# Kernel tuning notes

Measured on AMD Instinct MI355X. Metric: run time of the kernel, lower is better.

## Reference

```python
import jax, jax.numpy as jnp
import numpy as np

B, N, K, DIM = 1, 50000, 16, 64


def setup_inputs() -> dict:
    key = jax.random.key(0)
    ks = jax.random.split(key, 16)
    s = 0.05  # weight init scale
    return {
        "points_xyz": jax.random.normal(ks[0], (B, N, 3), jnp.float32),
        "points_features": jax.random.normal(ks[1], (B, N, DIM), jnp.float32),
        "neighbours_xyz": jax.random.normal(ks[2], (B, N, K, 3), jnp.float32),
        "neighbours_features": jax.random.normal(ks[3], (B, N, K, DIM), jnp.float32),
        "W_phi": jax.random.normal(ks[4], (DIM, DIM), jnp.float32) * s,
        "b_phi": jnp.zeros((DIM,), jnp.float32),
        "W_psi": jax.random.normal(ks[5], (DIM, DIM), jnp.float32) * s,
        "b_psi": jnp.zeros((DIM,), jnp.float32),
        "W_alpha": jax.random.normal(ks[6], (DIM, DIM), jnp.float32) * s,
        "b_alpha": jnp.zeros((DIM,), jnp.float32),
        "W_gamma": jax.random.normal(ks[7], (DIM, DIM), jnp.float32) * s,
        "b_gamma": jnp.zeros((DIM,), jnp.float32),
        "W_d1": jax.random.normal(ks[8], (3, DIM), jnp.float32) * s,
        "b_d1": jnp.zeros((DIM,), jnp.float32),
        "W_d2": jax.random.normal(ks[9], (DIM, DIM), jnp.float32) * s,
        "b_d2": jnp.zeros((DIM,), jnp.float32),
    }


def reference(points_xyz, points_features, neighbours_xyz, neighbours_features,
              W_phi, b_phi, W_psi, b_psi, W_alpha, b_alpha, W_gamma, b_gamma,
              W_d1, b_d1, W_d2, b_d2):
    # Positional encoding: delta(p_i - p_j) -> (B, N, K, DIM)
    diff = points_xyz[:, :, None, :] - neighbours_xyz          # (B,N,K,3)
    delta = jax.nn.relu((diff @ W_d1 + b_d1) @ W_d2 + b_d2)    # (B,N,K,DIM)

    phi = (points_features @ W_phi + b_phi)[:, :, None, :]     # (B,N,1,DIM)
    psi = neighbours_features @ W_psi + b_psi                  # (B,N,K,DIM)
    beta = phi - psi + delta                                   # (B,N,K,DIM)

    gamma_out = beta @ W_gamma + b_gamma                       # (B,N,K,DIM)
    # NOTE: faithful to source: softmax over the FEATURE axis (dim=-1)
    rho = jax.nn.softmax(gamma_out, axis=-1)                   # (B,N,K,DIM)

    alpha_out = neighbours_features @ W_alpha + b_alpha + delta  # (B,N,K,DIM)
    out = jnp.sum(rho * alpha_out, axis=2)                     # (B,N,DIM)
    return out
```

## Files before the change

### kernel.cpp

```cpp
#include <hip/hip_runtime.h>
#include <hip/hip_bf16.h>

typedef unsigned int uint_t;
typedef __attribute__((ext_vector_type(8))) short bf16x8;
typedef __attribute__((ext_vector_type(4))) float f32x4;

#define NPTS 50000
#define DIM  64
#define KNB  16
#define GPW  8
#define NGROUPS (NPTS / GPW)
#define WPB  4
#define NBLOCKS ((NGROUPS + WPB - 1) / WPB)

#define FR_WA    0
#define FR_PSIG  2048
#define FR_WG    4096
#define FR_PHIG  6144
#define WC4      8192
#define GB       8448
#define BA       8512

__device__ __forceinline__ uint_t pk(float a, float b) {
    union { __hip_bfloat162 h; uint_t u; } cv;
    cv.h = __float22bfloat162_rn(float2{a, b});
    return cv.u;
}

union Frag { uint_t u[4]; bf16x8 s; uint4 v; };

__device__ __forceinline__ int sigma(int k) {
    int t = k >> 1;
    return (t & 15) + 32 * (t >> 4) + 16 * (k & 1);
}

__global__ void pt_prep(const float* __restrict__ Wphi, const float* __restrict__ bphi,
                        const float* __restrict__ Wpsi, const float* __restrict__ bpsi,
                        const float* __restrict__ Wa,   const float* __restrict__ ba,
                        const float* __restrict__ Wg,   const float* __restrict__ bg,
                        const float* __restrict__ Wd1,  const float* __restrict__ bd1,
                        const float* __restrict__ Wd2,  const float* __restrict__ bd2,
                        float* __restrict__ ws) {
    int b = blockIdx.x, t = threadIdx.x;
    uint_t* wsu = (uint_t*)ws;
    if (b < 32) {
        int gid  = b * 256 + t;
        int img  = gid >> 11;
        int rem  = gid & 2047;
        int f    = rem >> 8;
        int lane = (rem >> 2) & 63;
        int w    = rem & 3;
        int k0   = (f & 1) * 32 + (lane >> 4) * 8 + 2 * w;
        int k1   = k0 + 1;
        int n    = (f >> 1) * 16 + (lane & 15);
        float v0, v1;
        if (img == 0) {
            v0 = Wa[k0 * 64 + n]; v1 = Wa[k1 * 64 + n];
            wsu[FR_WA + rem] = pk(v0, v1);
        } else if (img == 1) {
            float a0 = 0.f, a1 = 0.f;
            for (int c = 0; c < 64; ++c) {
                float wgc = Wg[c * 64 + n];
                a0 += Wpsi[k0 * 64 + c] * wgc;
                a1 += Wpsi[k1 * 64 + c] * wgc;
            }
            wsu[FR_PSIG + rem] = pk(-a0, -a1);
        } else if (img == 2) {
            v0 = Wg[sigma(k0) * 64 + n]; v1 = Wg[sigma(k1) * 64 + n];
            wsu[FR_WG + rem] = pk(v0, v1);
        } else {
            float a0 = 0.f, a1 = 0.f;
            for (int c = 0; c < 64; ++c) {
                float wgc = Wg[c * 64 + n];
                a0 += Wphi[k0 * 64 + c] * wgc;
                a1 += Wphi[k1 * 64 + c] * wgc;
            }
            wsu[FR_PHIG + rem] = pk(a0, a1);
        }
    } else if (t < 64) {
        float wx = 0.f, wy = 0.f, wz = 0.f;
        for (int m = 0; m < 64; ++m) {
            float w2 = Wd2[m * 64 + t];
            wx += Wd1[m] * w2;
            wy += Wd1[64 + m] * w2;
            wz += Wd1[128 + m] * w2;
        }
        float wb = bd2[t];
        for (int m = 0; m < 64; ++m) wb += bd1[m] * Wd2[m * 64 + t];
        ws[WC4 + t * 4 + 0] = wx;
        ws[WC4 + t * 4 + 1] = wy;
        ws[WC4 + t * 4 + 2] = wz;
        ws[WC4 + t * 4 + 3] = wb;
        float g = bg[t];
        for (int c = 0; c < 64; ++c) g += (bphi[c] - bpsi[c]) * Wg[c * 64 + t];
        ws[GB + t] = g;
        ws[BA + t] = ba[t];
    }
}

#define MFMA(A, B, C) __builtin_amdgcn_mfma_f32_16x16x32_bf16((A), (B), (C), 0, 0, 0)

#define O_PHIG 0
#define O_UTR  520
#define O_DXY  1064
#define O_PXY  1128
#define O_OBUF 1160
#define O_NF   1672
#define NFSLOT 1088
#define WAREA  (O_NF + 3 * NFSLOT)

__device__ __forceinline__ void gl_lds16(const void* g, void* l) {
    __builtin_amdgcn_global_load_lds(
        (const __attribute__((address_space(1))) unsigned int*)g,
        (__attribute__((address_space(3))) unsigned int*)l, 16, 0, 0);
}
__device__ __forceinline__ void gl_lds4(const void* g, void* l) {
    __builtin_amdgcn_global_load_lds(
        (const __attribute__((address_space(1))) unsigned int*)g,
        (__attribute__((address_space(3))) unsigned int*)l, 4, 0, 0);
}

__device__ __forceinline__ void stage_pt(const float* __restrict__ nfeat,
                                         const float* __restrict__ nxyz,
                                         int p, float* ldsbase,
                                         const int* soff, int lane) {
    const char* sp = (const char*)nfeat + (size_t)p * 4096;
    gl_lds16(sp + soff[0], ldsbase);
    gl_lds16(sp + soff[1], ldsbase + 256);
    gl_lds16(sp + soff[2], ldsbase + 512);
    gl_lds16(sp + soff[3], ldsbase + 768);
    int xi = p * 48 + lane;
    if (xi > NPTS * KNB * 3 - 1) xi = NPTS * KNB * 3 - 1;
    gl_lds4(nxyz + xi, ldsbase + 1024);
}

__global__ __launch_bounds__(256, 2)
void pt_main(const float* __restrict__ pxyz, const float* __restrict__ pfeat,
             const float* __restrict__ nxyz, const float* __restrict__ nfeat,
             const float* __restrict__ ws,   float* __restrict__ out) {
    __shared__ float lds[WPB][WAREA];

    const int t    = threadIdx.x;
    const int wv   = t >> 6;
    const int lane = t & 63;
    const int c16  = lane & 15;
    const int quad = lane >> 4;

    const int g = blockIdx.x * WPB + wv;
    if (g >= NGROUPS) return;

    float*  W      = lds[wv];
    float*  phig_s = W + O_PHIG;
    uint_t* utr    = (uint_t*)(W + O_UTR);
    float*  dxyz   = W + O_DXY;
    float*  pxyz_s = W + O_PXY;
    float*  obuf   = W + O_OBUF;
    float*  nfl    = W + O_NF;

    const int g0 = g * GPW;
    const int k3 = lane / 3, c3 = lane - k3 * 3;

    int soff[4];
    #pragma unroll
    for (int j = 0; j < 4; ++j) {
        int row = j * 4 + quad;
        soff[j] = row * 256 + (((c16 - row) & 15) << 4);
    }

    stage_pt(nfeat, nxyz, g0,     nfl + 0 * NFSLOT, soff, lane);
    stage_pt(nfeat, nxyz, g0 + 1, nfl + 1 * NFSLOT, soff, lane);

    const uint4* fr = (const uint4*)ws;
    Frag wa[8], wpsig[8], wg[8];
    #pragma unroll
    for (int f = 0; f < 8; ++f) {
        wa[f].v    = fr[        f * 64 + lane];
        wpsig[f].v = fr[ 512 +  f * 64 + lane];
        wg[f].v    = fr[1024 +  f * 64 + lane];
    }
    float4 wc[4];
    float ba_r[4], gbr[4];
    #pragma unroll
    for (int nt = 0; nt < 4; ++nt) {
        int d = nt * 16 + c16;
        wc[nt]   = ((const float4*)(ws + WC4))[d];
        ba_r[nt] = ws[BA + d];
        gbr[nt]  = ws[GB + d];
    }

    if (lane < 24) pxyz_s[lane] = pxyz[g0 * 3 + lane];

    {
        float4 x0{}, x1{}, x2{}, x3{};
        if (c16 < 8) {
            const float* base = pfeat + (size_t)(g0 + c16) * 64 + quad * 8;
            x0 = *(const float4*)(base);
            x1 = *(const float4*)(base + 4);
            x2 = *(const float4*)(base + 32);
            x3 = *(const float4*)(base + 36);
        }
        Frag pa0, pa1;
        pa0.u[0] = pk(x0.x, x0.y); pa0.u[1] = pk(x0.z, x0.w);
        pa0.u[2] = pk(x1.x, x1.y); pa0.u[3] = pk(x1.z, x1.w);
        pa1.u[0] = pk(x2.x, x2.y); pa1.u[1] = pk(x2.z, x2.w);
        pa1.u[2] = pk(x3.x, x3.y); pa1.u[3] = pk(x3.z, x3.w);
        #pragma unroll
        for (int nt = 0; nt < 4; ++nt) {
            Frag b0, b1;
            b0.v = fr[1536 + (nt * 2 + 0) * 64 + lane];
            b1.v = fr[1536 + (nt * 2 + 1) * 64 + lane];
            f32x4 acc = {gbr[nt], gbr[nt], gbr[nt], gbr[nt]};
            acc = MFMA(pa0.s, b0.s, acc);
            acc = MFMA(pa1.s, b1.s, acc);
            if (quad < 2) {
                #pragma unroll
                for (int r = 0; r < 4; ++r)
                    phig_s[(quad * 4 + r) * 65 + nt * 16 + c16] = acc[r];
            }
        }
    }

    int slot = 0;
    #pragma unroll 1
    for (int i = 0; i < GPW; ++i) {
        const int n = g0 + i;

        if (i + 2 < GPW) {
            int s2 = slot + 2; if (s2 >= 3) s2 -= 3;
            stage_pt(nfeat, nxyz, n + 2, nfl + s2 * NFSLOT, soff, lane);
        }
        __builtin_amdgcn_sched_barrier(0);
        if (i < GPW - 2)       { asm volatile("s_waitcnt vmcnt(10)" ::: "memory"); }
        else if (i == GPW - 2) { asm volatile("s_waitcnt vmcnt(5)"  ::: "memory"); }
        else                   { asm volatile("s_waitcnt vmcnt(0)"  ::: "memory"); }
        __builtin_amdgcn_sched_barrier(0);

        const float* nfp = nfl + slot * NFSLOT;

        if (lane < 48) {
            float v = nfp[1024 + lane];
            dxyz[k3 * 4 + c3] = pxyz_s[i * 3 + c3] - v;
        }

        int b0 = c16 * 64 + (((quad * 2     + c16) & 15) << 2);
        int b1 = c16 * 64 + (((quad * 2 + 1 + c16) & 15) << 2);
        int b2 = c16 * 64 + (((quad * 2 + 8 + c16) & 15) << 2);
        int b3 = c16 * 64 + (((quad * 2 + 9 + c16) & 15) << 2);
        float4 x0 = *(const float4*)(nfp + b0);
        float4 x1 = *(const float4*)(nfp + b1);
        float4 x2 = *(const float4*)(nfp + b2);
        float4 x3 = *(const float4*)(nfp + b3);
        Frag na0, na1;
        na0.u[0] = pk(x0.x, x0.y); na0.u[1] = pk(x0.z, x0.w);
        na0.u[2] = pk(x1.x, x1.y); na0.u[3] = pk(x1.z, x1.w);
        na1.u[0] = pk(x2.x, x2.y); na1.u[1] = pk(x2.z, x2.w);
        na1.u[2] = pk(x3.x, x3.y); na1.u[3] = pk(x3.z, x3.w);

        float ph[4];
        #pragma unroll
        for (int nt = 0; nt < 4; ++nt) ph[nt] = phig_s[i * 65 + nt * 16 + c16];
        float4 dd[4];
        #pragma unroll
        for (int r = 0; r < 4; ++r)
            dd[r] = ((const float4*)dxyz)[quad * 4 + r];

        float d_c[4][4];
        #pragma unroll
        for (int nt = 0; nt < 4; ++nt) {
            #pragma unroll
            for (int r = 0; r < 4; ++r) {
                float u = fmaf(dd[r].x, wc[nt].x,
                          fmaf(dd[r].y, wc[nt].y,
                          fmaf(dd[r].z, wc[nt].z, wc[nt].w)));
                d_c[nt][r] = fmaxf(u, 0.f);
            }
        }
        #pragma unroll
        for (int r = 0; r < 4; ++r) {
            int row = (quad * 4 + r) * 34;
            utr[row + c16]      = pk(d_c[0][r], d_c[1][r]);
            utr[row + 16 + c16] = pk(d_c[2][r], d_c[3][r]);
        }

        f32x4 aacc[4];
        #pragma unroll
        for (int nt = 0; nt < 4; ++nt) {
            aacc[nt] = f32x4{ba_r[nt], ba_r[nt], ba_r[nt], ba_r[nt]};
            aacc[nt] = MFMA(na0.s, wa[nt * 2 + 0].s, aacc[nt]);
            aacc[nt] = MFMA(na1.s, wa[nt * 2 + 1].s, aacc[nt]);
        }
        f32x4 gacc[4];
        #pragma unroll
        for (int nt = 0; nt < 4; ++nt) {
            gacc[nt] = f32x4{ph[nt], ph[nt], ph[nt], ph[nt]};
            gacc[nt] = MFMA(na0.s, wpsig[nt * 2 + 0].s, gacc[nt]);
            gacc[nt] = MFMA(na1.s, wpsig[nt * 2 + 1].s, gacc[nt]);
        }
        Frag da0, da1;
        {
            const uint_t* rowp = utr + c16 * 34 + quad * 4;
            uint2 a = *(const uint2*)(rowp);
            uint2 b = *(const uint2*)(rowp + 2);
            uint2 c = *(const uint2*)(rowp + 16);
            uint2 d = *(const uint2*)(rowp + 18);
            da0.u[0] = a.x; da0.u[1] = a.y; da0.u[2] = b.x; da0.u[3] = b.y;
            da1.u[0] = c.x; da1.u[1] = c.y; da1.u[2] = d.x; da1.u[3] = d.y;
        }
        #pragma unroll
        for (int nt = 0; nt < 4; ++nt) {
            gacc[nt] = MFMA(da0.s, wg[nt * 2 + 0].s, gacc[nt]);
            gacc[nt] = MFMA(da1.s, wg[nt * 2 + 1].s, gacc[nt]);
        }
        #pragma unroll
        for (int nt = 0; nt < 4; ++nt)
            #pragma unroll
            for (int r = 0; r < 4; ++r) aacc[nt][r] += d_c[nt][r];

        float e[4][4], smi[4];
        #pragma unroll
        for (int r = 0; r < 4; ++r) {
            float s = 0.f;
            #pragma unroll
            for (int nt = 0; nt < 4; ++nt) { e[nt][r] = __expf(gacc[nt][r]); s += e[nt][r]; }
            #pragma unroll
            for (int d2 = 1; d2 < 16; d2 <<= 1) s += __shfl_xor(s, d2);
            smi[r] = __builtin_amdgcn_rcpf(s);
        }
        float p0 = 0.f, p1 = 0.f, p2 = 0.f, p3 = 0.f;
        #pragma unroll
        for (int r = 0; r < 4; ++r) {
            p0 = fmaf(e[0][r] * smi[r], aacc[0][r], p0);
            p1 = fmaf(e[1][r] * smi[r], aacc[1][r], p1);
            p2 = fmaf(e[2][r] * smi[r], aacc[2][r], p2);
            p3 = fmaf(e[3][r] * smi[r], aacc[3][r], p3);
        }
        p0 += __shfl_xor(p0, 16); p0 += __shfl_xor(p0, 32);
        p1 += __shfl_xor(p1, 16); p1 += __shfl_xor(p1, 32);
        p2 += __shfl_xor(p2, 16); p2 += __shfl_xor(p2, 32);
        p3 += __shfl_xor(p3, 16); p3 += __shfl_xor(p3, 32);
        float sel = (quad == 0) ? p0 : (quad == 1) ? p1 : (quad == 2) ? p2 : p3;
        obuf[i * 64 + lane] = sel;

        slot = (slot == 2) ? 0 : slot + 1;
    }

    float4 o0 = ((const float4*)obuf)[lane * 2];
    float4 o1 = ((const float4*)obuf)[lane * 2 + 1];
    float4* og = (float4*)(out + (size_t)g0 * 64);
    og[lane * 2]     = o0;
    og[lane * 2 + 1] = o1;
}

extern "C" void kernel_launch(void* const* d_in, const int* in_sizes, int n_in,
                              void* d_out, int out_size, void* d_ws, size_t ws_size,
                              hipStream_t stream) {
    const float* pxyz  = (const float*)d_in[0];
    const float* pfeat = (const float*)d_in[1];
    const float* nxyz  = (const float*)d_in[2];
    const float* nfeat = (const float*)d_in[3];
    const float* Wphi  = (const float*)d_in[4];
    const float* bphi  = (const float*)d_in[5];
    const float* Wpsi  = (const float*)d_in[6];
    const float* bpsi  = (const float*)d_in[7];
    const float* Wa    = (const float*)d_in[8];
    const float* ba    = (const float*)d_in[9];
    const float* Wg    = (const float*)d_in[10];
    const float* bg    = (const float*)d_in[11];
    const float* Wd1   = (const float*)d_in[12];
    const float* bd1   = (const float*)d_in[13];
    const float* Wd2   = (const float*)d_in[14];
    const float* bd2   = (const float*)d_in[15];
    float* ws = (float*)d_ws;

    pt_prep<<<33, 256, 0, stream>>>(Wphi, bphi, Wpsi, bpsi, Wa, ba, Wg, bg,
                                    Wd1, bd1, Wd2, bd2, ws);
    pt_main<<<NBLOCKS, 256, 0, stream>>>(pxyz, pfeat, nxyz, nfeat, ws, (float*)d_out);
}
```

Measured before the change: 351.3 us.

## Replace async global-to-LDS triple buffering with register-staged double buffering

```diff
diff --git a/kernel.cpp b/kernel.cpp
--- a/kernel.cpp
+++ b/kernel.cpp
@@ -103,36 +103,10 @@
 #define O_PHIG 0
 #define O_UTR  520
 #define O_DXY  1064
-#define O_PXY  1128
-#define O_OBUF 1160
-#define O_NF   1672
-#define NFSLOT 1088
-#define WAREA  (O_NF + 3 * NFSLOT)
-
-__device__ __forceinline__ void gl_lds16(const void* g, void* l) {
-    __builtin_amdgcn_global_load_lds(
-        (const __attribute__((address_space(1))) unsigned int*)g,
-        (__attribute__((address_space(3))) unsigned int*)l, 16, 0, 0);
-}
-__device__ __forceinline__ void gl_lds4(const void* g, void* l) {
-    __builtin_amdgcn_global_load_lds(
-        (const __attribute__((address_space(1))) unsigned int*)g,
-        (__attribute__((address_space(3))) unsigned int*)l, 4, 0, 0);
-}
-
-__device__ __forceinline__ void stage_pt(const float* __restrict__ nfeat,
-                                         const float* __restrict__ nxyz,
-                                         int p, float* ldsbase,
-                                         const int* soff, int lane) {
-    const char* sp = (const char*)nfeat + (size_t)p * 4096;
-    gl_lds16(sp + soff[0], ldsbase);
-    gl_lds16(sp + soff[1], ldsbase + 256);
-    gl_lds16(sp + soff[2], ldsbase + 512);
-    gl_lds16(sp + soff[3], ldsbase + 768);
-    int xi = p * 48 + lane;
-    if (xi > NPTS * KNB * 3 - 1) xi = NPTS * KNB * 3 - 1;
-    gl_lds4(nxyz + xi, ldsbase + 1024);
-}
+#define O_PXY  1192
+#define O_OBUF 1224
+#define O_NF   1736
+#define WAREA  (O_NF + 2 * 1024)
 
 __global__ __launch_bounds__(256, 2)
 void pt_main(const float* __restrict__ pxyz, const float* __restrict__ pfeat,
@@ -167,8 +141,12 @@
         soff[j] = row * 256 + (((c16 - row) & 15) << 4);
     }
 
-    stage_pt(nfeat, nxyz, g0,     nfl + 0 * NFSLOT, soff, lane);
-    stage_pt(nfeat, nxyz, g0 + 1, nfl + 1 * NFSLOT, soff, lane);
+    const char* nfbase = (const char*)nfeat + (size_t)g0 * 4096;
+
+    float4 x[4];
+    #pragma unroll
+    for (int j = 0; j < 4; ++j)
+        x[j] = *(const float4*)(nfbase + soff[j]);
 
     const uint4* fr = (const uint4*)ws;
     Frag wa[8], wpsig[8], wg[8];
@@ -189,15 +167,23 @@
     }
 
     if (lane < 24) pxyz_s[lane] = pxyz[g0 * 3 + lane];
+    float nv0 = (lane < 48) ? nxyz[(size_t)g0 * 48 + lane] : 0.f;
+    if (lane < 48) dxyz[k3 * 4 + c3] = pxyz_s[c3] - nv0;
 
     {
+        float4* scr4 = (float4*)(W + O_UTR);
+        const float4* pfg4 = (const float4*)(pfeat + (size_t)g0 * 64);
+        if (lane < 32) {
+            #pragma unroll
+            for (int j = 0; j < 4; ++j)
+                scr4[j * 32 + lane] = pfg4[j * 32 + lane];
+        }
         float4 x0{}, x1{}, x2{}, x3{};
         if (c16 < 8) {
-            const float* base = pfeat + (size_t)(g0 + c16) * 64 + quad * 8;
-            x0 = *(const float4*)(base);
-            x1 = *(const float4*)(base + 4);
-            x2 = *(const float4*)(base + 32);
-            x3 = *(const float4*)(base + 36);
+            x0 = scr4[c16 * 16 + quad * 2];
+            x1 = scr4[c16 * 16 + quad * 2 + 1];
+            x2 = scr4[c16 * 16 + 8 + quad * 2];
+            x3 = scr4[c16 * 16 + 9 + quad * 2];
         }
         Frag pa0, pa1;
         pa0.u[0] = pk(x0.x, x0.y); pa0.u[1] = pk(x0.z, x0.w);
@@ -220,27 +206,32 @@
         }
     }
 
-    int slot = 0;
+    {
+        float4* s0 = (float4*)nfl;
+        #pragma unroll
+        for (int j = 0; j < 4; ++j) s0[j * 64 + lane] = x[j];
+    }
+    #pragma unroll
+    for (int j = 0; j < 4; ++j)
+        x[j] = *(const float4*)(nfbase + 4096 + soff[j]);
+    float nvn = (lane < 48) ? nxyz[(size_t)g0 * 48 + 48 + lane] : 0.f;
+
     #pragma unroll 1
     for (int i = 0; i < GPW; ++i) {
         const int n = g0 + i;
 
-        if (i + 2 < GPW) {
-            int s2 = slot + 2; if (s2 >= 3) s2 -= 3;
-            stage_pt(nfeat, nxyz, n + 2, nfl + s2 * NFSLOT, soff, lane);
-        }
-        __builtin_amdgcn_sched_barrier(0);
-        if (i < GPW - 2)       { asm volatile("s_waitcnt vmcnt(10)" ::: "memory"); }
-        else if (i == GPW - 2) { asm volatile("s_waitcnt vmcnt(5)"  ::: "memory"); }
-        else                   { asm volatile("s_waitcnt vmcnt(0)"  ::: "memory"); }
-        __builtin_amdgcn_sched_barrier(0);
-
-        const float* nfp = nfl + slot * NFSLOT;
-
-        if (lane < 48) {
-            float v = nfp[1024 + lane];
-            dxyz[k3 * 4 + c3] = pxyz_s[i * 3 + c3] - v;
-        }
+        if (i + 1 < GPW) {
+            float4* sw = (float4*)(nfl + ((i + 1) & 1) * 1024);
+            #pragma unroll
+            for (int j = 0; j < 4; ++j) sw[j * 64 + lane] = x[j];
+            if (i + 2 < GPW) {
+                #pragma unroll
+                for (int j = 0; j < 4; ++j)
+                    x[j] = *(const float4*)(nfbase + (size_t)(i + 2) * 4096 + soff[j]);
+            }
+        }
+
+        const float* nfp = nfl + (i & 1) * 1024;
 
         int b0 = c16 * 64 + (((quad * 2     + c16) & 15) << 2);
         int b1 = c16 * 64 + (((quad * 2 + 1 + c16) & 15) << 2);
@@ -262,7 +253,14 @@
         float4 dd[4];
         #pragma unroll
         for (int r = 0; r < 4; ++r)
-            dd[r] = ((const float4*)dxyz)[quad * 4 + r];
+            dd[r] = ((const float4*)dxyz)[(i & 1) * 16 + quad * 4 + r];
+
+        if (i + 1 < GPW) {
+            if (lane < 48)
+                dxyz[((i + 1) & 1) * 64 + k3 * 4 + c3] = pxyz_s[(i + 1) * 3 + c3] - nvn;
+            if (i + 2 < GPW)
+                nvn = (lane < 48) ? nxyz[((size_t)n + 2) * 48 + lane] : 0.f;
+        }
 
         float d_c[4][4];
         #pragma unroll
@@ -341,7 +339,6 @@
         float sel = (quad == 0) ? p0 : (quad == 1) ? p1 : (quad == 2) ? p2 : p3;
         obuf[i * 64 + lane] = sel;
 
-        slot = (slot == 2) ? 0 : slot + 1;
     }
 
     float4 o0 = ((const float4*)obuf)[lane * 2];
```

Result: slower. 377.9 us (+7.6%).
